# Kernel tuning notes

Measured on AMD Instinct MI355X. Metric: run time of the kernel, lower is better.

The kernel has to match this reference:

```python
import jax, jax.numpy as jnp
import numpy as np

B, N, C = 4, 2048, 768
H = 12
D = C // H  # 64

def setup_inputs() -> dict:
    key = jax.random.key(0)
    k1, k2, k3 = jax.random.split(key, 3)
    x = jax.random.normal(k1, (B, N, C), dtype=jnp.float32)
    qkv_w = jax.random.normal(k2, (3 * C, C), dtype=jnp.float32) * (C ** -0.5)
    proj_w = jax.random.normal(k3, (C, C), dtype=jnp.float32) * (C ** -0.5)
    return {"x": x, "qkv_w": qkv_w, "proj_w": proj_w}

def reference(x, qkv_w, proj_w):
    b, n, c = x.shape
    h, d = H, c // H
    # qkv projection (Linear, no bias): [B,N,3C] -> [3,B,H,N,D]
    qkv = jnp.einsum('bnc,fc->bnf', x, qkv_w)
    qkv = qkv.reshape(b, n, 3, h, d).transpose(2, 0, 3, 1, 4)
    q, k, v = qkv[0], qkv[1], qkv[2]
    # scaled dot-product attention; module divides by sqrt(head_dim)
    scale = 1.0 / jnp.sqrt(jnp.float32(d)).astype(x.dtype)
    score = jnp.einsum('bhqd,bhkd->bhqk', q, k) * scale  # [B,H,N,N] full matrix, as in source
    attn = jax.nn.softmax(score, axis=-1)
    ctx = jnp.einsum('bhqk,bhkd->bhqd', attn, v)
    ctx = ctx.transpose(0, 2, 1, 3).reshape(b, n, c)
    out = jnp.einsum('bnc,oc->bno', ctx, proj_w)  # proj Linear, no bias; dropout p=0
    return out
```

## Files before the change

### kernel.cpp

```cpp
#include <hip/hip_runtime.h>
#include <hip/hip_bf16.h>

#define BB 4
#define NN 2048
#define CC 768
#define HH 12
#define DD 64
#define MTOT (BB*NN)

typedef __attribute__((ext_vector_type(8))) short frag16;
typedef __attribute__((ext_vector_type(4))) float f32x4;
typedef __attribute__((ext_vector_type(16))) float f32x16;
typedef __attribute__((ext_vector_type(4))) unsigned int u32x4;

#if defined(__has_builtin)
#if __has_builtin(__builtin_amdgcn_permlane32_swap)
#define HAVE_PLSWAP 1
#endif
#endif

static __device__ __forceinline__ float bf2f(unsigned short u) {
  unsigned int x = ((unsigned int)u) << 16;
  return __builtin_bit_cast(float, x);
}
static __device__ __forceinline__ unsigned short f2bf(float f) {
  __hip_bfloat16 h = __float2bfloat16(f);
  return __builtin_bit_cast(unsigned short, h);
}
static __device__ __forceinline__ unsigned int cvt_pk_bf16(float lo, float hi) {
  unsigned int r;
  asm("v_cvt_pk_bf16_f32 %0, %1, %2" : "=v"(r) : "v"(lo), "v"(hi));
  return r;
}
static __device__ __forceinline__ void gload16(const void* g, void* l) {
  __builtin_amdgcn_global_load_lds((const __attribute__((address_space(1))) void*)g,
                                   (__attribute__((address_space(3))) void*)l, 16, 0, 0);
}

#define QSCALE 0.18033688011112042f

__global__ void detect_k(const unsigned short* x, int* flag) {
  __shared__ int cnt;
  if (threadIdx.x == 0) cnt = 0;
  __syncthreads();
  float v = bf2f(x[threadIdx.x]);
  float a = fabsf(v);
  int weird = (!(a <= 1e4f)) || (a != 0.0f && a < 1e-10f);
  if (weird) atomicAdd(&cnt, 1);
  __syncthreads();
  if (threadIdx.x == 0) *flag = (cnt >= 24) ? 1 : 0;
}

__global__ void conv3_k(const void* __restrict__ s0, const void* __restrict__ s1,
                        const void* __restrict__ s2,
                        unsigned short* __restrict__ d0, unsigned short* __restrict__ d1,
                        unsigned short* __restrict__ d2,
                        const int* __restrict__ flag) {
  if (!*flag) return;
  const int N0 = MTOT * CC, N1 = 3 * CC * CC, N2 = CC * CC;
  int i = (blockIdx.x * blockDim.x + threadIdx.x) * 4;
  int stride = gridDim.x * blockDim.x * 4;
  for (; i < N0 + N1 + N2; i += stride) {
    const float* s;
    unsigned short* d;
    int j = i;
    if (j < N0) { s = (const float*)s0; d = d0; }
    else if (j < N0 + N1) { j -= N0; s = (const float*)s1; d = d1; }
    else { j -= N0 + N1; s = (const float*)s2; d = d2; }
    float4 v = *reinterpret_cast<const float4*>(&s[j]);
    ushort4 o;
    o.x = f2bf(v.x); o.y = f2bf(v.y); o.z = f2bf(v.z); o.w = f2bf(v.w);
    *reinterpret_cast<ushort4*>(&d[j]) = o;
  }
}

template<int EPI, int BN>
__global__ __launch_bounds__(256) void gemm_bt(const unsigned short* __restrict__ Araw,
                                               const unsigned short* __restrict__ Aconv,
                                               const unsigned short* __restrict__ Braw,
                                               const unsigned short* __restrict__ Bconv,
                                               unsigned short* __restrict__ qkvbuf,
                                               void* __restrict__ outp,
                                               const int* __restrict__ flag) {
  constexpr int K = CC;
  constexpr int FN = BN / 32;
  __shared__ unsigned short Asm[2][128 * 32];
  __shared__ unsigned short Bsm[2][BN * 32];
  const int tid = threadIdx.x;
  const int lane = tid & 63;
  const int w = tid >> 6;
  const int wm = w >> 1, wn = w & 1;
  const int l15 = lane & 15;
  const int g = lane >> 4;
  const int m0 = blockIdx.x * 128;
  const int f0 = blockIdx.y * BN;
  const int fp32 = *flag;

  const unsigned short* A = fp32 ? Aconv : Araw;
  const unsigned short* Bw = fp32 ? Bconv : Braw;

  f32x4 acc[4][FN];
#pragma unroll
  for (int i = 0; i < 4; ++i)
#pragma unroll
    for (int j = 0; j < FN; ++j) acc[i][j] = (f32x4){0.f, 0.f, 0.f, 0.f};

  const unsigned short* Abase = A + (size_t)m0 * K;
  const unsigned short* Bbase = Bw + (size_t)f0 * K;

#define GSTAGE(buf, k0)                                                               \
  {                                                                                   \
    _Pragma("unroll")                                                                 \
    for (int i_ = 0; i_ < 2; ++i_) {                                                  \
      int chunk = (i_ * 4 + w) * 64 + lane;                                           \
      int row = chunk >> 2;                                                           \
      int col = (chunk & 3) << 3;                                                     \
      gload16(Abase + (size_t)row * K + (k0) + col,                                   \
              (char*)&Asm[buf][0] + (i_ * 4 + w) * 1024);                             \
    }                                                                                 \
    if constexpr (BN == 128) {                                                        \
      _Pragma("unroll")                                                               \
      for (int i_ = 0; i_ < 2; ++i_) {                                                \
        int chunk = (i_ * 4 + w) * 64 + lane;                                         \
        int row = chunk >> 2;                                                         \
        int col = (chunk & 3) << 3;                                                   \
        gload16(Bbase + (size_t)row * K + (k0) + col,                                 \
                (char*)&Bsm[buf][0] + (i_ * 4 + w) * 1024);                           \
      }                                                                               \
    } else {                                                                          \
      int chunk = w * 64 + lane;                                                      \
      int row = chunk >> 2;                                                           \
      int col = (chunk & 3) << 3;                                                     \
      gload16(Bbase + (size_t)row * K + (k0) + col,                                   \
              (char*)&Bsm[buf][0] + w * 1024 + lane * 16);                            \
    }                                                                                 \
  }

  int cur = 0;
  GSTAGE(0, 0)

  for (int kt = 0; kt < K / 32; ++kt) {
    __syncthreads();
    if (kt + 1 < K / 32) GSTAGE(cur ^ 1, (kt + 1) * 32)

    frag16 af[4], bfv[FN];
#pragma unroll
    for (int t = 0; t < 4; ++t)
      af[t] = *reinterpret_cast<const frag16*>(&Asm[cur][(wm * 64 + t * 16 + l15) * 32 + 8 * g]);
#pragma unroll
    for (int t = 0; t < FN; ++t)
      bfv[t] = *reinterpret_cast<const frag16*>(
          &Bsm[cur][(wn * (BN / 2) + t * 16 + l15) * 32 + 8 * g]);
    __builtin_amdgcn_s_setprio(1);
#pragma unroll
    for (int i = 0; i < 4; ++i)
#pragma unroll
      for (int j = 0; j < FN; ++j)
        acc[i][j] = __builtin_amdgcn_mfma_f32_16x16x32_bf16(af[i], bfv[j], acc[i][j], 0, 0, 0);
    __builtin_amdgcn_s_setprio(0);
    cur ^= 1;
  }
#undef GSTAGE

  if constexpr (EPI == 0) {
    const size_t plane = (size_t)BB * HH * NN * DD;
#pragma unroll
    for (int i = 0; i < 4; ++i) {
      int mbase = m0 + wm * 64 + i * 16 + 4 * g;
#pragma unroll
      for (int j = 0; j < FN; ++j) {
        int f = f0 + wn * (BN / 2) + j * 16 + l15;
        int which = f / CC;
        int rem = f - which * CC;
        int h = rem >> 6, d = rem & 63;
        if (which == 2) {
          int b = mbase >> 11, n = mbase & 2047;
          int nsw = (n & ~63) | ((n & 63) ^ ((d & 7) << 3));
          ushort4 o;
#pragma unroll
          for (int r = 0; r < 4; ++r) ((unsigned short*)&o)[r] = f2bf(acc[i][j][r]);
          size_t idx = 2 * plane + (((size_t)(b * HH + h) * DD + d) * NN + nsw);
          *reinterpret_cast<ushort4*>(&qkvbuf[idx]) = o;
        } else if (which == 1) {
#pragma unroll
          for (int r = 0; r < 4; ++r) {
            int mm = mbase + r;
            int b = mm >> 11, n = mm & 2047;
            int dsw = d ^ ((n & 7) << 3);
            size_t idx = plane + (((size_t)(b * HH + h) * NN + n) * DD + dsw);
            qkvbuf[idx] = f2bf(acc[i][j][r]);
          }
        } else {
#pragma unroll
          for (int r = 0; r < 4; ++r) {
            int mm = mbase + r;
            int b = mm >> 11, n = mm & 2047;
            size_t idx = (((size_t)(b * HH + h) * NN + n) * DD + d);
            qkvbuf[idx] = f2bf(acc[i][j][r] * QSCALE);
          }
        }
      }
    }
  } else {
    int ofp32 = fp32;
#pragma unroll
    for (int i = 0; i < 4; ++i) {
      int mbase = m0 + wm * 64 + i * 16 + 4 * g;
#pragma unroll
      for (int j = 0; j < FN; ++j) {
        int f = f0 + wn * (BN / 2) + j * 16 + l15;
#pragma unroll
        for (int r = 0; r < 4; ++r) {
          size_t idx = (size_t)(mbase + r) * CC + f;
          if (ofp32) ((float*)outp)[idx] = acc[i][j][r];
          else ((unsigned short*)outp)[idx] = f2bf(acc[i][j][r]);
        }
      }
    }
  }
}

template<int SPLIT>
__global__ __launch_bounds__(512) void attn_k(const unsigned short* __restrict__ qkv,
                                              unsigned short* __restrict__ outp,
                                              float* __restrict__ ml) {
  __shared__ unsigned short Kb[2][64 * 64];
  __shared__ unsigned short Vb[2][64 * 64];
  const int tid = threadIdx.x;
  const int lane = tid & 63;
  const int w = tid >> 6;
  const int l31 = lane & 31;
  const int hl = lane >> 5;

  int orig = blockIdx.x;
  int sp, bh, q0, kvbeg, kvend;
  if constexpr (SPLIT) {
    int wgid = (orig & 7) * 96 + (orig >> 3);
    sp = wgid / 384;
    int rem = wgid - sp * 384;
    bh = rem >> 3;
    q0 = (rem & 7) * 256;
    kvbeg = sp * 16;
    kvend = kvbeg + 16;
  } else {
    int wgid = (orig & 7) * 48 + (orig >> 3);
    sp = 0;
    bh = wgid >> 3;
    q0 = (wgid & 7) * 256;
    kvbeg = 0;
    kvend = NN / 64;
  }

  const size_t plane = (size_t)BB * HH * NN * DD;
  const unsigned short* Qg = qkv + (size_t)bh * NN * DD;
  const unsigned short* Kg = qkv + plane + (size_t)bh * NN * DD;
  const unsigned short* Vt = qkv + 2 * plane + (size_t)bh * NN * DD;

  frag16 qb[4];
  {
    int qrow = q0 + w * 32 + l31;
#pragma unroll
    for (int s = 0; s < 4; ++s)
      qb[s] = *reinterpret_cast<const frag16*>(&Qg[(size_t)qrow * DD + s * 16 + hl * 8]);
  }

  f32x16 acc0, acc1;
#pragma unroll
  for (int i = 0; i < 16; ++i) { acc0[i] = 0.f; acc1[i] = 0.f; }
  float lsum = 0.f;

  const int srow = tid >> 3;
  const int scol = (tid & 7) * 8;
#define STAGE(buf, n0)                                                   \
  {                                                                      \
    gload16(Kg + (size_t)((n0) + srow) * DD + scol, &Kb[buf][tid * 8]);  \
    gload16(Vt + (size_t)srow * NN + (n0) + scol, &Vb[buf][tid * 8]);    \
  }

  int cur = 0;
  STAGE(0, kvbeg * 64)

  for (int kv = kvbeg; kv < kvend; ++kv) {
    __syncthreads();
    if (kv + 1 < kvend) STAGE(cur ^ 1, (kv + 1) * 64)

    const char* Kc = (const char*)&Kb[cur][0];
    const char* Vc = (const char*)&Vb[cur][0];
    const int xk = (l31 & 7) << 4;

    f32x16 s0, s1;
#pragma unroll
    for (int i = 0; i < 16; ++i) { s0[i] = 0.f; s1[i] = 0.f; }
    __builtin_amdgcn_s_setprio(1);
#pragma unroll
    for (int s = 0; s < 4; ++s) {
      frag16 ka = *reinterpret_cast<const frag16*>(
          Kc + (l31) * 128 + (((s * 16 + hl * 8) * 2) ^ xk));
      s0 = __builtin_amdgcn_mfma_f32_32x32x16_bf16(ka, qb[s], s0, 0, 0, 0);
    }
#pragma unroll
    for (int s = 0; s < 4; ++s) {
      frag16 ka = *reinterpret_cast<const frag16*>(
          Kc + (32 + l31) * 128 + (((s * 16 + hl * 8) * 2) ^ xk));
      s1 = __builtin_amdgcn_mfma_f32_32x32x16_bf16(ka, qb[s], s1, 0, 0, 0);
    }
    __builtin_amdgcn_s_setprio(0);

#pragma unroll
    for (int r = 0; r < 16; ++r) s0[r] = __builtin_amdgcn_exp2f(s0[r]);
#pragma unroll
    for (int r = 0; r < 16; ++r) s1[r] = __builtin_amdgcn_exp2f(s1[r]);
    {
      float a0 = s0[0] + s1[0], a1 = s0[1] + s1[1], a2 = s0[2] + s1[2], a3 = s0[3] + s1[3];
#pragma unroll
      for (int r = 4; r < 16; r += 4) {
        a0 += s0[r] + s1[r];
        a1 += s0[r + 1] + s1[r + 1];
        a2 += s0[r + 2] + s1[r + 2];
        a3 += s0[r + 3] + s1[r + 3];
      }
      float tot = (a0 + a1) + (a2 + a3);
      tot += __shfl_xor(tot, 32);
      lsum += tot;
    }

    frag16 pA0, pA1, pB0, pB1;
#ifdef HAVE_PLSWAP
    {
      unsigned int wv[8];
#pragma unroll
      for (int i = 0; i < 8; ++i) wv[i] = cvt_pk_bf16(s0[2 * i], s0[2 * i + 1]);
      auto r02 = __builtin_amdgcn_permlane32_swap(wv[0], wv[2], false, false);
      auto r13 = __builtin_amdgcn_permlane32_swap(wv[1], wv[3], false, false);
      auto r46 = __builtin_amdgcn_permlane32_swap(wv[4], wv[6], false, false);
      auto r57 = __builtin_amdgcn_permlane32_swap(wv[5], wv[7], false, false);
      u32x4 f0v = {(unsigned int)r02[0], (unsigned int)r13[0], (unsigned int)r02[1], (unsigned int)r13[1]};
      u32x4 f1v = {(unsigned int)r46[0], (unsigned int)r57[0], (unsigned int)r46[1], (unsigned int)r57[1]};
      pA0 = __builtin_bit_cast(frag16, f0v);
      pA1 = __builtin_bit_cast(frag16, f1v);
    }
    {
      unsigned int wv[8];
#pragma unroll
      for (int i = 0; i < 8; ++i) wv[i] = cvt_pk_bf16(s1[2 * i], s1[2 * i + 1]);
      auto r02 = __builtin_amdgcn_permlane32_swap(wv[0], wv[2], false, false);
      auto r13 = __builtin_amdgcn_permlane32_swap(wv[1], wv[3], false, false);
      auto r46 = __builtin_amdgcn_permlane32_swap(wv[4], wv[6], false, false);
      auto r57 = __builtin_amdgcn_permlane32_swap(wv[5], wv[7], false, false);
      u32x4 f0v = {(unsigned int)r02[0], (unsigned int)r13[0], (unsigned int)r02[1], (unsigned int)r13[1]};
      u32x4 f1v = {(unsigned int)r46[0], (unsigned int)r57[0], (unsigned int)r46[1], (unsigned int)r57[1]};
      pB0 = __builtin_bit_cast(frag16, f0v);
      pB1 = __builtin_bit_cast(frag16, f1v);
    }
#else
    {
      unsigned int wv[8], xw[8];
#pragma unroll
      for (int i = 0; i < 8; ++i) wv[i] = cvt_pk_bf16(s0[2 * i], s0[2 * i + 1]);
#pragma unroll
      for (int i = 0; i < 8; ++i) xw[i] = (unsigned int)__shfl_xor((int)wv[i], 32);
      u32x4 f0v = {hl ? xw[2] : wv[0], hl ? xw[3] : wv[1], hl ? wv[2] : xw[0], hl ? wv[3] : xw[1]};
      u32x4 f1v = {hl ? xw[6] : wv[4], hl ? xw[7] : wv[5], hl ? wv[6] : xw[4], hl ? wv[7] : xw[5]};
      pA0 = __builtin_bit_cast(frag16, f0v);
      pA1 = __builtin_bit_cast(frag16, f1v);
    }
    {
      unsigned int wv[8], xw[8];
#pragma unroll
      for (int i = 0; i < 8; ++i) wv[i] = cvt_pk_bf16(s1[2 * i], s1[2 * i + 1]);
#pragma unroll
      for (int i = 0; i < 8; ++i) xw[i] = (unsigned int)__shfl_xor((int)wv[i], 32);
      u32x4 f0v = {hl ? xw[2] : wv[0], hl ? xw[3] : wv[1], hl ? wv[2] : xw[0], hl ? wv[3] : xw[1]};
      u32x4 f1v = {hl ? xw[6] : wv[4], hl ? xw[7] : wv[5], hl ? wv[6] : xw[4], hl ? wv[7] : xw[5]};
      pB0 = __builtin_bit_cast(frag16, f0v);
      pB1 = __builtin_bit_cast(frag16, f1v);
    }
#endif

    __builtin_amdgcn_s_setprio(1);
#pragma unroll
    for (int dh = 0; dh < 2; ++dh) {
      f32x16& a = dh ? acc1 : acc0;
      frag16 vb;
      vb = *reinterpret_cast<const frag16*>(
          Vc + (dh * 32 + l31) * 128 + (((hl * 8) * 2) ^ xk));
      a = __builtin_amdgcn_mfma_f32_32x32x16_bf16(pA0, vb, a, 0, 0, 0);
      vb = *reinterpret_cast<const frag16*>(
          Vc + (dh * 32 + l31) * 128 + (((16 + hl * 8) * 2) ^ xk));
      a = __builtin_amdgcn_mfma_f32_32x32x16_bf16(pA1, vb, a, 0, 0, 0);
      vb = *reinterpret_cast<const frag16*>(
          Vc + (dh * 32 + l31) * 128 + (((32 + hl * 8) * 2) ^ xk));
      a = __builtin_amdgcn_mfma_f32_32x32x16_bf16(pB0, vb, a, 0, 0, 0);
      vb = *reinterpret_cast<const frag16*>(
          Vc + (dh * 32 + l31) * 128 + (((32 + 16 + hl * 8) * 2) ^ xk));
      a = __builtin_amdgcn_mfma_f32_32x32x16_bf16(pB1, vb, a, 0, 0, 0);
    }
    __builtin_amdgcn_s_setprio(0);
    cur ^= 1;
  }

  float inv = 1.0f / lsum;
  if constexpr (SPLIT) {
    size_t rowbase = ((size_t)(sp * (BB * HH) + bh) * NN + q0 + w * 32);
#pragma unroll
    for (int r = 0; r < 16; ++r) {
      int qr = (r & 3) + 8 * (r >> 2) + 4 * hl;
      float ivr = __shfl(inv, qr);
      size_t base = (rowbase + qr) * DD;
      outp[base + l31] = f2bf(acc0[r] * ivr);
      outp[base + 32 + l31] = f2bf(acc1[r] * ivr);
    }
    if (hl == 0) {
      size_t mlrow = (size_t)sp * (BB * HH * NN) + (size_t)bh * NN + q0 + w * 32 + l31;
      ml[mlrow] = lsum;
    }
  } else {
    const int b = bh / HH, h = bh - b * HH;
#pragma unroll
    for (int r = 0; r < 16; ++r) {
      int qr = (r & 3) + 8 * (r >> 2) + 4 * hl;
      float ivr = __shfl(inv, qr);
      int qn = q0 + w * 32 + qr;
      size_t base = ((size_t)(b * NN + qn)) * CC + h * DD;
      outp[base + l31] = f2bf(acc0[r] * ivr);
      outp[base + 32 + l31] = f2bf(acc1[r] * ivr);
    }
  }
#undef STAGE
}

__global__ __launch_bounds__(256) void combine_k(const unsigned short* __restrict__ ctxp,
                                                 const float* __restrict__ ml,
                                                 unsigned short* __restrict__ ctx) {
  const int tid = threadIdx.x;
  const int row = blockIdx.x * 32 + (tid >> 3);
  const int d0 = (tid & 7) * 8;
  const size_t PL = (size_t)BB * HH * NN * DD;
  const size_t MLP = (size_t)BB * HH * NN;
  float l0 = ml[row], l1 = ml[MLP + row];
  float inv = 1.0f / (l0 + l1);
  float w0 = l0 * inv, w1 = l1 * inv;
  u32x4 a = *reinterpret_cast<const u32x4*>(&ctxp[(size_t)row * DD + d0]);
  u32x4 bq = *reinterpret_cast<const u32x4*>(&ctxp[PL + (size_t)row * DD + d0]);
  const unsigned short* ap = (const unsigned short*)&a;
  const unsigned short* bp = (const unsigned short*)&bq;
  ushort4 o[2];
#pragma unroll
  for (int j = 0; j < 8; ++j)
    ((unsigned short*)o)[j] = f2bf(w0 * bf2f(ap[j]) + w1 * bf2f(bp[j]));
  const int bh = row >> 11, q = row & 2047;
  const int b = bh / HH, h = bh - b * HH;
  size_t base = ((size_t)(b * NN + q)) * CC + h * DD + d0;
  *reinterpret_cast<u32x4*>(&ctx[base]) = *reinterpret_cast<u32x4*>(&o[0]);
}

extern "C" void kernel_launch(void* const* d_in, const int* in_sizes, int n_in,
                              void* d_out, int out_size, void* d_ws, size_t ws_size,
                              hipStream_t stream) {
  const void* x = d_in[0];
  const void* qw = d_in[1];
  const void* pw = d_in[2];
  char* ws = (char*)d_ws;
  int* flag = (int*)ws;
  size_t off = 256;
  unsigned short* xb = (unsigned short*)(ws + off); off += (size_t)MTOT * CC * 2;
  unsigned short* qwb = (unsigned short*)(ws + off); off += (size_t)3 * CC * CC * 2;
  unsigned short* pwb = (unsigned short*)(ws + off); off += (size_t)CC * CC * 2;
  unsigned short* qkvbuf = (unsigned short*)(ws + off); off += (size_t)3 * MTOT * CC * 2;
  unsigned short* ctxp = (unsigned short*)(ws + off);
  size_t off2 = off + (size_t)2 * BB * HH * NN * DD * 2;
  float* ml = (float*)(ws + off2);
  size_t need = off2 + (size_t)2 * BB * HH * NN * 4;
  unsigned short* ctx = xb;

  detect_k<<<1, 256, 0, stream>>>((const unsigned short*)x, flag);
  conv3_k<<<2048, 256, 0, stream>>>(x, qw, pw, xb, qwb, pwb, flag);
  gemm_bt<0, 128><<<dim3(MTOT / 128, (3 * CC) / 128), 256, 0, stream>>>(
      (const unsigned short*)x, xb, (const unsigned short*)qw, qwb, qkvbuf, nullptr, flag);
  if (ws_size >= need) {
    attn_k<1><<<768, 512, 0, stream>>>(qkvbuf, ctxp, ml);
    combine_k<<<3072, 256, 0, stream>>>(ctxp, ml, ctx);
  } else {
    attn_k<0><<<384, 512, 0, stream>>>(qkvbuf, ctx, nullptr);
  }
  gemm_bt<1, 64><<<dim3(MTOT / 128, CC / 64), 256, 0, stream>>>(
      ctx, ctx, (const unsigned short*)pw, pwb, nullptr, d_out, flag);
}
```

Before: 145.0 us.

## Process 64 query rows per wave in attention, halving waves per block

Each attention wave now handles two 32-row query tiles instead of one, and the block shrinks from 512 to 256 threads. Each K and V fragment loaded from shared memory is reused for both query tiles, which halves LDS read traffic per MFMA and processes the KV tile in two 32-key sub-steps. The cost is roughly double the accumulator and Q registers per wave, which may lower occupancy, and fewer waves per block to hide the staging loads.

```diff
diff --git a/kernel.cpp b/kernel.cpp
--- a/kernel.cpp
+++ b/kernel.cpp
@@ -221,7 +221,7 @@
 }
 
 template<int SPLIT>
-__global__ __launch_bounds__(512) void attn_k(const unsigned short* __restrict__ qkv,
+__global__ __launch_bounds__(256) void attn_k(const unsigned short* __restrict__ qkv,
                                               unsigned short* __restrict__ outp,
                                               float* __restrict__ ml) {
   __shared__ unsigned short Kb[2][64 * 64];
@@ -256,25 +256,31 @@
   const unsigned short* Kg = qkv + plane + (size_t)bh * NN * DD;
   const unsigned short* Vt = qkv + 2 * plane + (size_t)bh * NN * DD;
 
-  frag16 qb[4];
+  frag16 qbA[4], qbB[4];
   {
-    int qrow = q0 + w * 32 + l31;
-#pragma unroll
-    for (int s = 0; s < 4; ++s)
-      qb[s] = *reinterpret_cast<const frag16*>(&Qg[(size_t)qrow * DD + s * 16 + hl * 8]);
-  }
-
-  f32x16 acc0, acc1;
-#pragma unroll
-  for (int i = 0; i < 16; ++i) { acc0[i] = 0.f; acc1[i] = 0.f; }
-  float lsum = 0.f;
-
-  const int srow = tid >> 3;
-  const int scol = (tid & 7) * 8;
-#define STAGE(buf, n0)                                                   \
-  {                                                                      \
-    gload16(Kg + (size_t)((n0) + srow) * DD + scol, &Kb[buf][tid * 8]);  \
-    gload16(Vt + (size_t)srow * NN + (n0) + scol, &Vb[buf][tid * 8]);    \
+    int qrow = q0 + w * 64 + l31;
+#pragma unroll
+    for (int s = 0; s < 4; ++s) {
+      qbA[s] = *reinterpret_cast<const frag16*>(&Qg[(size_t)qrow * DD + s * 16 + hl * 8]);
+      qbB[s] = *reinterpret_cast<const frag16*>(&Qg[(size_t)(qrow + 32) * DD + s * 16 + hl * 8]);
+    }
+  }
+
+  f32x16 accA0, accA1, accB0, accB1;
+#pragma unroll
+  for (int i = 0; i < 16; ++i) { accA0[i] = 0.f; accA1[i] = 0.f; accB0[i] = 0.f; accB1[i] = 0.f; }
+  float lsumA = 0.f, lsumB = 0.f;
+
+#define STAGE(buf, n0)                                                              \
+  {                                                                                 \
+    _Pragma("unroll")                                                               \
+    for (int i_ = 0; i_ < 2; ++i_) {                                                \
+      int c_ = i_ * 256 + tid;                                                      \
+      int r_ = c_ >> 3;                                                             \
+      int co_ = (c_ & 7) * 8;                                                       \
+      gload16(Kg + (size_t)((n0) + r_) * DD + co_, &Kb[buf][c_ * 8]);               \
+      gload16(Vt + (size_t)r_ * NN + (n0) + co_, &Vb[buf][c_ * 8]);                 \
+    }                                                                               \
   }
 
   int cur = 0;
@@ -288,142 +294,159 @@
     const char* Vc = (const char*)&Vb[cur][0];
     const int xk = (l31 & 7) << 4;
 
-    f32x16 s0, s1;
-#pragma unroll
-    for (int i = 0; i < 16; ++i) { s0[i] = 0.f; s1[i] = 0.f; }
-    __builtin_amdgcn_s_setprio(1);
-#pragma unroll
-    for (int s = 0; s < 4; ++s) {
-      frag16 ka = *reinterpret_cast<const frag16*>(
-          Kc + (l31) * 128 + (((s * 16 + hl * 8) * 2) ^ xk));
-      s0 = __builtin_amdgcn_mfma_f32_32x32x16_bf16(ka, qb[s], s0, 0, 0, 0);
-    }
-#pragma unroll
-    for (int s = 0; s < 4; ++s) {
-      frag16 ka = *reinterpret_cast<const frag16*>(
-          Kc + (32 + l31) * 128 + (((s * 16 + hl * 8) * 2) ^ xk));
-      s1 = __builtin_amdgcn_mfma_f32_32x32x16_bf16(ka, qb[s], s1, 0, 0, 0);
-    }
-    __builtin_amdgcn_s_setprio(0);
-
-#pragma unroll
-    for (int r = 0; r < 16; ++r) s0[r] = __builtin_amdgcn_exp2f(s0[r]);
-#pragma unroll
-    for (int r = 0; r < 16; ++r) s1[r] = __builtin_amdgcn_exp2f(s1[r]);
-    {
-      float a0 = s0[0] + s1[0], a1 = s0[1] + s1[1], a2 = s0[2] + s1[2], a3 = s0[3] + s1[3];
-#pragma unroll
-      for (int r = 4; r < 16; r += 4) {
-        a0 += s0[r] + s1[r];
-        a1 += s0[r + 1] + s1[r + 1];
-        a2 += s0[r + 2] + s1[r + 2];
-        a3 += s0[r + 3] + s1[r + 3];
-      }
-      float tot = (a0 + a1) + (a2 + a3);
-      tot += __shfl_xor(tot, 32);
-      lsum += tot;
-    }
-
-    frag16 pA0, pA1, pB0, pB1;
+#pragma unroll
+    for (int sub = 0; sub < 2; ++sub) {
+      frag16 ka[4];
+#pragma unroll
+      for (int s = 0; s < 4; ++s)
+        ka[s] = *reinterpret_cast<const frag16*>(
+            Kc + (sub * 32 + l31) * 128 + (((s * 16 + hl * 8) * 2) ^ xk));
+      f32x16 sA, sB;
+#pragma unroll
+      for (int i = 0; i < 16; ++i) { sA[i] = 0.f; sB[i] = 0.f; }
+      __builtin_amdgcn_s_setprio(1);
+#pragma unroll
+      for (int s = 0; s < 4; ++s)
+        sA = __builtin_amdgcn_mfma_f32_32x32x16_bf16(ka[s], qbA[s], sA, 0, 0, 0);
+#pragma unroll
+      for (int s = 0; s < 4; ++s)
+        sB = __builtin_amdgcn_mfma_f32_32x32x16_bf16(ka[s], qbB[s], sB, 0, 0, 0);
+      __builtin_amdgcn_s_setprio(0);
+
+#pragma unroll
+      for (int r = 0; r < 16; ++r) sA[r] = __builtin_amdgcn_exp2f(sA[r]);
+#pragma unroll
+      for (int r = 0; r < 16; ++r) sB[r] = __builtin_amdgcn_exp2f(sB[r]);
+      {
+        float a0 = sA[0], a1 = sA[1], a2 = sA[2], a3 = sA[3];
+        float b0 = sB[0], b1 = sB[1], b2 = sB[2], b3 = sB[3];
+#pragma unroll
+        for (int r = 4; r < 16; r += 4) {
+          a0 += sA[r]; a1 += sA[r + 1]; a2 += sA[r + 2]; a3 += sA[r + 3];
+          b0 += sB[r]; b1 += sB[r + 1]; b2 += sB[r + 2]; b3 += sB[r + 3];
+        }
+        lsumA += (a0 + a1) + (a2 + a3);
+        lsumB += (b0 + b1) + (b2 + b3);
+      }
+
+      frag16 pA0, pA1, pB0, pB1;
 #ifdef HAVE_PLSWAP
-    {
-      unsigned int wv[8];
-#pragma unroll
-      for (int i = 0; i < 8; ++i) wv[i] = cvt_pk_bf16(s0[2 * i], s0[2 * i + 1]);
-      auto r02 = __builtin_amdgcn_permlane32_swap(wv[0], wv[2], false, false);
-      auto r13 = __builtin_amdgcn_permlane32_swap(wv[1], wv[3], false, false);
-      auto r46 = __builtin_amdgcn_permlane32_swap(wv[4], wv[6], false, false);
-      auto r57 = __builtin_amdgcn_permlane32_swap(wv[5], wv[7], false, false);
-      u32x4 f0v = {(unsigned int)r02[0], (unsigned int)r13[0], (unsigned int)r02[1], (unsigned int)r13[1]};
-      u32x4 f1v = {(unsigned int)r46[0], (unsigned int)r57[0], (unsigned int)r46[1], (unsigned int)r57[1]};
-      pA0 = __builtin_bit_cast(frag16, f0v);
-      pA1 = __builtin_bit_cast(frag16, f1v);
-    }
-    {
-      unsigned int wv[8];
-#pragma unroll
-      for (int i = 0; i < 8; ++i) wv[i] = cvt_pk_bf16(s1[2 * i], s1[2 * i + 1]);
-      auto r02 = __builtin_amdgcn_permlane32_swap(wv[0], wv[2], false, false);
-      auto r13 = __builtin_amdgcn_permlane32_swap(wv[1], wv[3], false, false);
-      auto r46 = __builtin_amdgcn_permlane32_swap(wv[4], wv[6], false, false);
-      auto r57 = __builtin_amdgcn_permlane32_swap(wv[5], wv[7], false, false);
-      u32x4 f0v = {(unsigned int)r02[0], (unsigned int)r13[0], (unsigned int)r02[1], (unsigned int)r13[1]};
-      u32x4 f1v = {(unsigned int)r46[0], (unsigned int)r57[0], (unsigned int)r46[1], (unsigned int)r57[1]};
-      pB0 = __builtin_bit_cast(frag16, f0v);
-      pB1 = __builtin_bit_cast(frag16, f1v);
-    }
+      {
+        unsigned int wv[8];
+#pragma unroll
+        for (int i = 0; i < 8; ++i) wv[i] = cvt_pk_bf16(sA[2 * i], sA[2 * i + 1]);
+        auto r02 = __builtin_amdgcn_permlane32_swap(wv[0], wv[2], false, false);
+        auto r13 = __builtin_amdgcn_permlane32_swap(wv[1], wv[3], false, false);
+        auto r46 = __builtin_amdgcn_permlane32_swap(wv[4], wv[6], false, false);
+        auto r57 = __builtin_amdgcn_permlane32_swap(wv[5], wv[7], false, false);
+        u32x4 f0v = {(unsigned int)r02[0], (unsigned int)r13[0], (unsigned int)r02[1], (unsigned int)r13[1]};
+        u32x4 f1v = {(unsigned int)r46[0], (unsigned int)r57[0], (unsigned int)r46[1], (unsigned int)r57[1]};
+        pA0 = __builtin_bit_cast(frag16, f0v);
+        pA1 = __builtin_bit_cast(frag16, f1v);
+      }
+      {
+        unsigned int wv[8];
+#pragma unroll
+        for (int i = 0; i < 8; ++i) wv[i] = cvt_pk_bf16(sB[2 * i], sB[2 * i + 1]);
+        auto r02 = __builtin_amdgcn_permlane32_swap(wv[0], wv[2], false, false);
+        auto r13 = __builtin_amdgcn_permlane32_swap(wv[1], wv[3], false, false);
+        auto r46 = __builtin_amdgcn_permlane32_swap(wv[4], wv[6], false, false);
+        auto r57 = __builtin_amdgcn_permlane32_swap(wv[5], wv[7], false, false);
+        u32x4 f0v = {(unsigned int)r02[0], (unsigned int)r13[0], (unsigned int)r02[1], (unsigned int)r13[1]};
+        u32x4 f1v = {(unsigned int)r46[0], (unsigned int)r57[0], (unsigned int)r46[1], (unsigned int)r57[1]};
+        pB0 = __builtin_bit_cast(frag16, f0v);
+        pB1 = __builtin_bit_cast(frag16, f1v);
+      }
 #else
-    {
-      unsigned int wv[8], xw[8];
-#pragma unroll
-      for (int i = 0; i < 8; ++i) wv[i] = cvt_pk_bf16(s0[2 * i], s0[2 * i + 1]);
-#pragma unroll
-      for (int i = 0; i < 8; ++i) xw[i] = (unsigned int)__shfl_xor((int)wv[i], 32);
-      u32x4 f0v = {hl ? xw[2] : wv[0], hl ? xw[3] : wv[1], hl ? wv[2] : xw[0], hl ? wv[3] : xw[1]};
-      u32x4 f1v = {hl ? xw[6] : wv[4], hl ? xw[7] : wv[5], hl ? wv[6] : xw[4], hl ? wv[7] : xw[5]};
-      pA0 = __builtin_bit_cast(frag16, f0v);
-      pA1 = __builtin_bit_cast(frag16, f1v);
-    }
-    {
-      unsigned int wv[8], xw[8];
-#pragma unroll
-      for (int i = 0; i < 8; ++i) wv[i] = cvt_pk_bf16(s1[2 * i], s1[2 * i + 1]);
-#pragma unroll
-      for (int i = 0; i < 8; ++i) xw[i] = (unsigned int)__shfl_xor((int)wv[i], 32);
-      u32x4 f0v = {hl ? xw[2] : wv[0], hl ? xw[3] : wv[1], hl ? wv[2] : xw[0], hl ? wv[3] : xw[1]};
-      u32x4 f1v = {hl ? xw[6] : wv[4], hl ? xw[7] : wv[5], hl ? wv[6] : xw[4], hl ? wv[7] : xw[5]};
-      pB0 = __builtin_bit_cast(frag16, f0v);
-      pB1 = __builtin_bit_cast(frag16, f1v);
-    }
+      {
+        unsigned int wv[8], xw[8];
+#pragma unroll
+        for (int i = 0; i < 8; ++i) wv[i] = cvt_pk_bf16(sA[2 * i], sA[2 * i + 1]);
+#pragma unroll
+        for (int i = 0; i < 8; ++i) xw[i] = (unsigned int)__shfl_xor((int)wv[i], 32);
+        u32x4 f0v = {hl ? xw[2] : wv[0], hl ? xw[3] : wv[1], hl ? wv[2] : xw[0], hl ? wv[3] : xw[1]};
+        u32x4 f1v = {hl ? xw[6] : wv[4], hl ? xw[7] : wv[5], hl ? wv[6] : xw[4], hl ? wv[7] : xw[5]};
+        pA0 = __builtin_bit_cast(frag16, f0v);
+        pA1 = __builtin_bit_cast(frag16, f1v);
+      }
+      {
+        unsigned int wv[8], xw[8];
+#pragma unroll
+        for (int i = 0; i < 8; ++i) wv[i] = cvt_pk_bf16(sB[2 * i], sB[2 * i + 1]);
+#pragma unroll
+        for (int i = 0; i < 8; ++i) xw[i] = (unsigned int)__shfl_xor((int)wv[i], 32);
+        u32x4 f0v = {hl ? xw[2] : wv[0], hl ? xw[3] : wv[1], hl ? wv[2] : xw[0], hl ? wv[3] : xw[1]};
+        u32x4 f1v = {hl ? xw[6] : wv[4], hl ? xw[7] : wv[5], hl ? wv[6] : xw[4], hl ? wv[7] : xw[5]};
+        pB0 = __builtin_bit_cast(frag16, f0v);
+        pB1 = __builtin_bit_cast(frag16, f1v);
+      }
 #endif
 
-    __builtin_amdgcn_s_setprio(1);
-#pragma unroll
-    for (int dh = 0; dh < 2; ++dh) {
-      f32x16& a = dh ? acc1 : acc0;
-      frag16 vb;
-      vb = *reinterpret_cast<const frag16*>(
-          Vc + (dh * 32 + l31) * 128 + (((hl * 8) * 2) ^ xk));
-      a = __builtin_amdgcn_mfma_f32_32x32x16_bf16(pA0, vb, a, 0, 0, 0);
-      vb = *reinterpret_cast<const frag16*>(
-          Vc + (dh * 32 + l31) * 128 + (((16 + hl * 8) * 2) ^ xk));
-      a = __builtin_amdgcn_mfma_f32_32x32x16_bf16(pA1, vb, a, 0, 0, 0);
-      vb = *reinterpret_cast<const frag16*>(
-          Vc + (dh * 32 + l31) * 128 + (((32 + hl * 8) * 2) ^ xk));
-      a = __builtin_amdgcn_mfma_f32_32x32x16_bf16(pB0, vb, a, 0, 0, 0);
-      vb = *reinterpret_cast<const frag16*>(
-          Vc + (dh * 32 + l31) * 128 + (((32 + 16 + hl * 8) * 2) ^ xk));
-      a = __builtin_amdgcn_mfma_f32_32x32x16_bf16(pB1, vb, a, 0, 0, 0);
-    }
-    __builtin_amdgcn_s_setprio(0);
+      __builtin_amdgcn_s_setprio(1);
+      {
+        frag16 vb0 = *reinterpret_cast<const frag16*>(
+            Vc + (l31) * 128 + (((sub * 32 + hl * 8) * 2) ^ xk));
+        frag16 vb1 = *reinterpret_cast<const frag16*>(
+            Vc + (l31) * 128 + (((sub * 32 + 16 + hl * 8) * 2) ^ xk));
+        accA0 = __builtin_amdgcn_mfma_f32_32x32x16_bf16(pA0, vb0, accA0, 0, 0, 0);
+        accA0 = __builtin_amdgcn_mfma_f32_32x32x16_bf16(pA1, vb1, accA0, 0, 0, 0);
+        accB0 = __builtin_amdgcn_mfma_f32_32x32x16_bf16(pB0, vb0, accB0, 0, 0, 0);
+        accB0 = __builtin_amdgcn_mfma_f32_32x32x16_bf16(pB1, vb1, accB0, 0, 0, 0);
+      }
+      {
+        frag16 vb0 = *reinterpret_cast<const frag16*>(
+            Vc + (32 + l31) * 128 + (((sub * 32 + hl * 8) * 2) ^ xk));
+        frag16 vb1 = *reinterpret_cast<const frag16*>(
+            Vc + (32 + l31) * 128 + (((sub * 32 + 16 + hl * 8) * 2) ^ xk));
+        accA1 = __builtin_amdgcn_mfma_f32_32x32x16_bf16(pA0, vb0, accA1, 0, 0, 0);
+        accA1 = __builtin_amdgcn_mfma_f32_32x32x16_bf16(pA1, vb1, accA1, 0, 0, 0);
+        accB1 = __builtin_amdgcn_mfma_f32_32x32x16_bf16(pB0, vb0, accB1, 0, 0, 0);
+        accB1 = __builtin_amdgcn_mfma_f32_32x32x16_bf16(pB1, vb1, accB1, 0, 0, 0);
+      }
+      __builtin_amdgcn_s_setprio(0);
+    }
     cur ^= 1;
   }
 
-  float inv = 1.0f / lsum;
+  lsumA += __shfl_xor(lsumA, 32);
+  lsumB += __shfl_xor(lsumB, 32);
+  float invA = 1.0f / lsumA;
+  float invB = 1.0f / lsumB;
+
   if constexpr (SPLIT) {
-    size_t rowbase = ((size_t)(sp * (BB * HH) + bh) * NN + q0 + w * 32);
+    size_t rowbase = ((size_t)(sp * (BB * HH) + bh) * NN + q0 + w * 64);
 #pragma unroll
     for (int r = 0; r < 16; ++r) {
       int qr = (r & 3) + 8 * (r >> 2) + 4 * hl;
-      float ivr = __shfl(inv, qr);
-      size_t base = (rowbase + qr) * DD;
-      outp[base + l31] = f2bf(acc0[r] * ivr);
-      outp[base + 32 + l31] = f2bf(acc1[r] * ivr);
+      float ivrA = __shfl(invA, qr);
+      float ivrB = __shfl(invB, qr);
+      size_t baseA = (rowbase + qr) * DD;
+      size_t baseB = (rowbase + 32 + qr) * DD;
+      outp[baseA + l31] = f2bf(accA0[r] * ivrA);
+      outp[baseA + 32 + l31] = f2bf(accA1[r] * ivrA);
+      outp[baseB + l31] = f2bf(accB0[r] * ivrB);
+      outp[baseB + 32 + l31] = f2bf(accB1[r] * ivrB);
     }
     if (hl == 0) {
-      size_t mlrow = (size_t)sp * (BB * HH * NN) + (size_t)bh * NN + q0 + w * 32 + l31;
-      ml[mlrow] = lsum;
+      size_t mlrow = (size_t)sp * (BB * HH * NN) + (size_t)bh * NN + q0 + w * 64 + l31;
+      ml[mlrow] = lsumA;
+      ml[mlrow + 32] = lsumB;
     }
   } else {
     const int b = bh / HH, h = bh - b * HH;
 #pragma unroll
     for (int r = 0; r < 16; ++r) {
       int qr = (r & 3) + 8 * (r >> 2) + 4 * hl;
-      float ivr = __shfl(inv, qr);
-      int qn = q0 + w * 32 + qr;
-      size_t base = ((size_t)(b * NN + qn)) * CC + h * DD;
-      outp[base + l31] = f2bf(acc0[r] * ivr);
-      outp[base + 32 + l31] = f2bf(acc1[r] * ivr);
+      float ivrA = __shfl(invA, qr);
+      float ivrB = __shfl(invB, qr);
+      int qnA = q0 + w * 64 + qr;
+      int qnB = qnA + 32;
+      size_t baseA = ((size_t)(b * NN + qnA)) * CC + h * DD;
+      size_t baseB = ((size_t)(b * NN + qnB)) * CC + h * DD;
+      outp[baseA + l31] = f2bf(accA0[r] * ivrA);
+      outp[baseA + 32 + l31] = f2bf(accA1[r] * ivrA);
+      outp[baseB + l31] = f2bf(accB0[r] * ivrB);
+      outp[baseB + 32 + l31] = f2bf(accB1[r] * ivrB);
     }
   }
 #undef STAGE
@@ -478,10 +501,10 @@
   gemm_bt<0, 128><<<dim3(MTOT / 128, (3 * CC) / 128), 256, 0, stream>>>(
       (const unsigned short*)x, xb, (const unsigned short*)qw, qwb, qkvbuf, nullptr, flag);
   if (ws_size >= need) {
-    attn_k<1><<<768, 512, 0, stream>>>(qkvbuf, ctxp, ml);
+    attn_k<1><<<768, 256, 0, stream>>>(qkvbuf, ctxp, ml);
     combine_k<<<3072, 256, 0, stream>>>(ctxp, ml, ctx);
   } else {
-    attn_k<0><<<384, 512, 0, stream>>>(qkvbuf, ctx, nullptr);
+    attn_k<0><<<384, 256, 0, stream>>>(qkvbuf, ctx, nullptr);
   }
   gemm_bt<1, 64><<<dim3(MTOT / 128, CC / 64), 256, 0, stream>>>(
       ctx, ctx, (const unsigned short*)pw, pwb, nullptr, d_out, flag);
```

Result: slower. 151.5 us (+4.5%).
